# Performance work log

Hardware: AMD Instinct MI355X
Metric: run time of the kernel (lower is better)

## Reference

```python
import jax, jax.numpy as jnp
import numpy as np

CHANNELS = 256   # input_channels == output_channels == res_feature channels
HIDDEN = 128
NODES = 7

def setup_inputs() -> dict:
    key = jax.random.key(0)
    k1, k2, k3, k4, k5 = jax.random.split(key, 5)
    batch, d, h, w = 2, 16, 64, 64
    inp = jax.random.normal(k1, (1, batch, NODES, HIDDEN), dtype=jnp.float32)
    res_feature = jax.random.normal(k2, (batch, CHANNELS, d, h, w), dtype=jnp.float32)
    # xavier_uniform-style init
    def xavier(k, shape):
        fan_in, fan_out = shape[0], shape[1]
        a = jnp.sqrt(6.0 / (fan_in + fan_out))
        return jax.random.uniform(k, shape, dtype=jnp.float32, minval=-a, maxval=a)
    node_fea_for_res = xavier(k3, (CHANNELS, NODES))
    node_fea_for_hidden = xavier(k4, (HIDDEN, 1))
    weight = xavier(k5, (HIDDEN, CHANNELS))
    return {"inp": inp, "res_feature": res_feature,
            "node_fea_for_res": node_fea_for_res,
            "node_fea_for_hidden": node_fea_for_hidden,
            "weight": weight}

def reference(inp, res_feature, node_fea_for_res, node_fea_for_hidden, weight):
    b, c, d, h, w = res_feature.shape
    # [b, dhw, c]
    rf = res_feature.reshape(b, c, d * h * w).transpose(0, 2, 1)
    # scores from residual features: [b, dhw, nodes]
    n1 = rf @ node_fea_for_res
    # scores from node hidden features (constant over spatial dim): [b, nodes]
    # (original expands input over dhw then matmuls with [hidden,1]; equivalent)
    n2 = (inp[0] @ node_fea_for_hidden)[..., 0]
    attn = jax.nn.softmax(n1 + n2[:, None, :], axis=-1)  # [b, dhw, nodes]
    new_weight = inp[0] @ weight                          # [b, nodes, c]
    feature_out = jnp.einsum('bpn,bnc->bpc', attn, new_weight)  # [b, dhw, c]
    feature_out = feature_out.transpose(0, 2, 1).reshape(b, c, d, h, w)
    return jax.nn.relu(feature_out)
```

## Files before the change

kernel.cpp:

```cpp
#include <hip/hip_runtime.h>

#define DHW    65536
#define NCH    256
#define NNODE  7
#define NHID   128
#define NBATCH 2

__global__ void prep_kernel(const float* __restrict__ inp,
                            const float* __restrict__ nfh,
                            const float* __restrict__ weight,
                            const float* __restrict__ w1,
                            float* __restrict__ nwt,
                            float* __restrict__ n2g,
                            float* __restrict__ w1p)
{
    const int bn = blockIdx.x;
    const int b  = bn / NNODE;
    const int n  = bn % NNODE;
    const int t  = threadIdx.x;
    const float* ih = inp + (b * NNODE + n) * NHID;

    float acc = 0.f;
    #pragma unroll 8
    for (int h = 0; h < NHID; ++h)
        acc = fmaf(ih[h], weight[h * NCH + t], acc);
    nwt[(b * NCH + t) * 8 + n] = acc;

    if (bn == 0) {
        #pragma unroll
        for (int n2 = 0; n2 < NNODE; ++n2) w1p[t * 8 + n2] = w1[t * NNODE + n2];
        w1p[t * 8 + 7] = 0.f;
    }

    __shared__ float red[NHID];
    if (t < NHID) red[t] = ih[t] * nfh[t];
    __syncthreads();
    for (int s = NHID / 2; s > 0; s >>= 1) {
        if (t < s) red[t] += red[t + s];
        __syncthreads();
    }
    if (t == 0) n2g[b * 8 + n] = red[0];
}

__global__ __launch_bounds__(256, 8)
void main_kernel(const float* __restrict__ rf,
                 const float* __restrict__ w1p,
                 const float* __restrict__ nwt,
                 const float* __restrict__ n2g,
                 float* __restrict__ out)
{
    __shared__ float red[8][4][64];

    const int t    = threadIdx.x;
    const int lane = t & 63;
    const int wv   = __builtin_amdgcn_readfirstlane(t >> 6);
    const int blk  = blockIdx.x;
    const int b    = blk >> 10;
    const int p    = ((blk & 1023) << 6) + lane;
    const int c0   = wv << 6;

    const float*  rp = rf + ((size_t)b << 24) + ((size_t)c0 << 16) + p;
    const float4* wq = (const float4*)w1p + (c0 << 1);

    float s0 = 0.f, s1 = 0.f, s2 = 0.f, s3 = 0.f, s4 = 0.f, s5 = 0.f, s6 = 0.f;
    #pragma unroll 8
    for (int c = 0; c < 64; ++c) {
        float  v  = rp[(size_t)c << 16];
        float4 wa = wq[c * 2];
        float4 wb = wq[c * 2 + 1];
        s0 = fmaf(v, wa.x, s0);
        s1 = fmaf(v, wa.y, s1);
        s2 = fmaf(v, wa.z, s2);
        s3 = fmaf(v, wa.w, s3);
        s4 = fmaf(v, wb.x, s4);
        s5 = fmaf(v, wb.y, s5);
        s6 = fmaf(v, wb.z, s6);
    }

    red[0][wv][lane] = s0;  red[1][wv][lane] = s1;  red[2][wv][lane] = s2;
    red[3][wv][lane] = s3;  red[4][wv][lane] = s4;  red[5][wv][lane] = s5;
    red[6][wv][lane] = s6;
    __syncthreads();

    const float* n2 = n2g + b * 8;
    float r0 = red[0][0][lane] + red[0][1][lane] + red[0][2][lane] + red[0][3][lane] + n2[0];
    float r1 = red[1][0][lane] + red[1][1][lane] + red[1][2][lane] + red[1][3][lane] + n2[1];
    float r2 = red[2][0][lane] + red[2][1][lane] + red[2][2][lane] + red[2][3][lane] + n2[2];
    float r3 = red[3][0][lane] + red[3][1][lane] + red[3][2][lane] + red[3][3][lane] + n2[3];
    float r4 = red[4][0][lane] + red[4][1][lane] + red[4][2][lane] + red[4][3][lane] + n2[4];
    float r5 = red[5][0][lane] + red[5][1][lane] + red[5][2][lane] + red[5][3][lane] + n2[5];
    float r6 = red[6][0][lane] + red[6][1][lane] + red[6][2][lane] + red[6][3][lane] + n2[6];

    float m = fmaxf(fmaxf(fmaxf(r0, r1), fmaxf(r2, r3)),
                    fmaxf(fmaxf(r4, r5), r6));
    float e0 = __expf(r0 - m), e1 = __expf(r1 - m), e2 = __expf(r2 - m);
    float e3 = __expf(r3 - m), e4 = __expf(r4 - m), e5 = __expf(r5 - m);
    float e6 = __expf(r6 - m);
    float inv = 1.0f / (e0 + e1 + e2 + e3 + e4 + e5 + e6);
    float a0 = e0 * inv, a1 = e1 * inv, a2 = e2 * inv, a3 = e3 * inv;
    float a4 = e4 * inv, a5 = e5 * inv, a6 = e6 * inv;

    const float4* nq = (const float4*)nwt + ((b * NCH + c0) << 1);
    float* op = out + ((size_t)b << 24) + ((size_t)c0 << 16) + p;
    #pragma unroll 8
    for (int c = 0; c < 64; ++c) {
        float4 na = nq[c * 2];
        float4 nb = nq[c * 2 + 1];
        float o = a0 * na.x + a1 * na.y + a2 * na.z + a3 * na.w
                + a4 * nb.x + a5 * nb.y + a6 * nb.z;
        op[(size_t)c << 16] = fmaxf(o, 0.f);
    }
}

extern "C" void kernel_launch(void* const* d_in, const int* in_sizes, int n_in,
                              void* d_out, int out_size, void* d_ws, size_t ws_size,
                              hipStream_t stream) {
    const float* inp = (const float*)d_in[0];
    const float* rf  = (const float*)d_in[1];
    const float* w1  = (const float*)d_in[2];
    const float* nfh = (const float*)d_in[3];
    const float* wgt = (const float*)d_in[4];
    float* out = (float*)d_out;

    float* nwt = (float*)d_ws;
    float* n2g = nwt + NBATCH * NCH * 8;
    float* w1p = n2g + NBATCH * 8;

    prep_kernel<<<NBATCH * NNODE, 256, 0, stream>>>(inp, nfh, wgt, w1, nwt, n2g, w1p);
    main_kernel<<<NBATCH * 1024, 256, 0, stream>>>(rf, w1p, nwt, n2g, out);
}
```

Measured before the change: 266.2 us.

## Split fused kernel into score, softmax and output passes with float4 access

The single fused kernel, which reduced per-pixel scores across channel waves in shared memory, is replaced by three kernels. One computes partial node scores per channel chunk into a global buffer, one reduces them and applies the softmax into an attention buffer, and one writes the output. All kernels use float4 loads and stores, with each thread handling 4 pixels. This adds roughly 2x extra intermediate global traffic (partials plus attention, about 6 MB written and read) and two more launches, in exchange for wider memory accesses and no block-level synchronisation.

```diff
diff --git a/kernel.cpp b/kernel.cpp
--- a/kernel.cpp
+++ b/kernel.cpp
@@ -5,6 +5,30 @@
 #define NNODE  7
 #define NHID   128
 #define NBATCH 2
+#define CCH    64
+#define NCC    4
+#define PTILE  1024
+
+__device__ inline float4 f4fma(float4 v, float w, float4 a) {
+    a.x = fmaf(v.x, w, a.x); a.y = fmaf(v.y, w, a.y);
+    a.z = fmaf(v.z, w, a.z); a.w = fmaf(v.w, w, a.w);
+    return a;
+}
+__device__ inline float4 f4max(float4 a, float4 b) {
+    return make_float4(fmaxf(a.x,b.x), fmaxf(a.y,b.y), fmaxf(a.z,b.z), fmaxf(a.w,b.w));
+}
+__device__ inline float4 f4expsub(float4 a, float4 m) {
+    return make_float4(__expf(a.x-m.x), __expf(a.y-m.y), __expf(a.z-m.z), __expf(a.w-m.w));
+}
+__device__ inline float4 f4add(float4 a, float4 b) {
+    return make_float4(a.x+b.x, a.y+b.y, a.z+b.z, a.w+b.w);
+}
+__device__ inline float4 f4mul(float4 a, float4 b) {
+    return make_float4(a.x*b.x, a.y*b.y, a.z*b.z, a.w*b.w);
+}
+__device__ inline float4 f4relu(float4 a) {
+    return make_float4(fmaxf(a.x,0.f), fmaxf(a.y,0.f), fmaxf(a.z,0.f), fmaxf(a.w,0.f));
+}
 
 __global__ void prep_kernel(const float* __restrict__ inp,
                             const float* __restrict__ nfh,
@@ -28,7 +52,7 @@
 
     if (bn == 0) {
         #pragma unroll
-        for (int n2 = 0; n2 < NNODE; ++n2) w1p[t * 8 + n2] = w1[t * NNODE + n2];
+        for (int k = 0; k < NNODE; ++k) w1p[t * 8 + k] = w1[t * NNODE + k];
         w1p[t * 8 + 7] = 0.f;
     }
 
@@ -42,73 +66,112 @@
     if (t == 0) n2g[b * 8 + n] = red[0];
 }
 
-__global__ __launch_bounds__(256, 8)
-void main_kernel(const float* __restrict__ rf,
-                 const float* __restrict__ w1p,
-                 const float* __restrict__ nwt,
-                 const float* __restrict__ n2g,
-                 float* __restrict__ out)
+__global__ __launch_bounds__(256, 2)
+void score_kernel(const float* __restrict__ rf,
+                  const float* __restrict__ w1p,
+                  float* __restrict__ partial)
 {
-    __shared__ float red[8][4][64];
+    const int blk = blockIdx.x;
+    const int pc  = blk & 63;
+    const int cc  = (blk >> 6) & (NCC - 1);
+    const int b   = blk >> 8;
+    const int t   = threadIdx.x;
+    const int i4  = pc * 256 + t;
+    const int c0  = cc * CCH;
 
-    const int t    = threadIdx.x;
-    const int lane = t & 63;
-    const int wv   = __builtin_amdgcn_readfirstlane(t >> 6);
-    const int blk  = blockIdx.x;
-    const int b    = blk >> 10;
-    const int p    = ((blk & 1023) << 6) + lane;
-    const int c0   = wv << 6;
-
-    const float*  rp = rf + ((size_t)b << 24) + ((size_t)c0 << 16) + p;
+    const float4* rp = (const float4*)rf + (((size_t)(b * NCH + c0)) << 14) + i4;
     const float4* wq = (const float4*)w1p + (c0 << 1);
 
-    float s0 = 0.f, s1 = 0.f, s2 = 0.f, s3 = 0.f, s4 = 0.f, s5 = 0.f, s6 = 0.f;
+    float4 a0 = {0,0,0,0}, a1 = {0,0,0,0}, a2 = {0,0,0,0}, a3 = {0,0,0,0};
+    float4 a4 = {0,0,0,0}, a5 = {0,0,0,0}, a6 = {0,0,0,0};
+
     #pragma unroll 8
-    for (int c = 0; c < 64; ++c) {
-        float  v  = rp[(size_t)c << 16];
-        float4 wa = wq[c * 2];
-        float4 wb = wq[c * 2 + 1];
-        s0 = fmaf(v, wa.x, s0);
-        s1 = fmaf(v, wa.y, s1);
-        s2 = fmaf(v, wa.z, s2);
-        s3 = fmaf(v, wa.w, s3);
-        s4 = fmaf(v, wb.x, s4);
-        s5 = fmaf(v, wb.y, s5);
-        s6 = fmaf(v, wb.z, s6);
+    for (int ci = 0; ci < CCH; ++ci) {
+        float4 v  = rp[(size_t)ci << 14];
+        float4 wa = wq[ci * 2];
+        float4 wb = wq[ci * 2 + 1];
+        a0 = f4fma(v, wa.x, a0);
+        a1 = f4fma(v, wa.y, a1);
+        a2 = f4fma(v, wa.z, a2);
+        a3 = f4fma(v, wa.w, a3);
+        a4 = f4fma(v, wb.x, a4);
+        a5 = f4fma(v, wb.y, a5);
+        a6 = f4fma(v, wb.z, a6);
     }
 
-    red[0][wv][lane] = s0;  red[1][wv][lane] = s1;  red[2][wv][lane] = s2;
-    red[3][wv][lane] = s3;  red[4][wv][lane] = s4;  red[5][wv][lane] = s5;
-    red[6][wv][lane] = s6;
-    __syncthreads();
+    float4* pp = (float4*)partial + (((b * NCC + cc) * 8) << 14) + i4;
+    pp[0 << 14] = a0;  pp[1 << 14] = a1;  pp[2 << 14] = a2;  pp[3 << 14] = a3;
+    pp[4 << 14] = a4;  pp[5 << 14] = a5;  pp[6 << 14] = a6;
+}
 
-    const float* n2 = n2g + b * 8;
-    float r0 = red[0][0][lane] + red[0][1][lane] + red[0][2][lane] + red[0][3][lane] + n2[0];
-    float r1 = red[1][0][lane] + red[1][1][lane] + red[1][2][lane] + red[1][3][lane] + n2[1];
-    float r2 = red[2][0][lane] + red[2][1][lane] + red[2][2][lane] + red[2][3][lane] + n2[2];
-    float r3 = red[3][0][lane] + red[3][1][lane] + red[3][2][lane] + red[3][3][lane] + n2[3];
-    float r4 = red[4][0][lane] + red[4][1][lane] + red[4][2][lane] + red[4][3][lane] + n2[4];
-    float r5 = red[5][0][lane] + red[5][1][lane] + red[5][2][lane] + red[5][3][lane] + n2[5];
-    float r6 = red[6][0][lane] + red[6][1][lane] + red[6][2][lane] + red[6][3][lane] + n2[6];
+__global__ void softmax_kernel(const float* __restrict__ partial,
+                               const float* __restrict__ n2g,
+                               float* __restrict__ attn)
+{
+    const int g  = blockIdx.x * 256 + threadIdx.x;
+    const int b  = g >> 14;
+    const int i4 = g & 16383;
 
-    float m = fmaxf(fmaxf(fmaxf(r0, r1), fmaxf(r2, r3)),
-                    fmaxf(fmaxf(r4, r5), r6));
-    float e0 = __expf(r0 - m), e1 = __expf(r1 - m), e2 = __expf(r2 - m);
-    float e3 = __expf(r3 - m), e4 = __expf(r4 - m), e5 = __expf(r5 - m);
-    float e6 = __expf(r6 - m);
-    float inv = 1.0f / (e0 + e1 + e2 + e3 + e4 + e5 + e6);
-    float a0 = e0 * inv, a1 = e1 * inv, a2 = e2 * inv, a3 = e3 * inv;
-    float a4 = e4 * inv, a5 = e5 * inv, a6 = e6 * inv;
+    const float4* pp = (const float4*)partial + (((size_t)b * NCC * 8) << 14) + i4;
+    const float*  n2 = n2g + b * 8;
+
+    float4 s[NNODE];
+    #pragma unroll
+    for (int n = 0; n < NNODE; ++n) {
+        float4 acc = make_float4(n2[n], n2[n], n2[n], n2[n]);
+        #pragma unroll
+        for (int cc = 0; cc < NCC; ++cc)
+            acc = f4add(acc, pp[(size_t)((cc * 8 + n)) << 14]);
+        s[n] = acc;
+    }
+    float4 m = s[0];
+    #pragma unroll
+    for (int n = 1; n < NNODE; ++n) m = f4max(m, s[n]);
+    float4 e[NNODE];
+    float4 sum = {0,0,0,0};
+    #pragma unroll
+    for (int n = 0; n < NNODE; ++n) { e[n] = f4expsub(s[n], m); sum = f4add(sum, e[n]); }
+    float4 inv = make_float4(1.f/sum.x, 1.f/sum.y, 1.f/sum.z, 1.f/sum.w);
+
+    float4* ap = (float4*)attn + (((size_t)b * 8) << 14) + i4;
+    #pragma unroll
+    for (int n = 0; n < NNODE; ++n) ap[(size_t)n << 14] = f4mul(e[n], inv);
+}
+
+__global__ __launch_bounds__(256, 2)
+void out_kernel(const float* __restrict__ attn,
+                const float* __restrict__ nwt,
+                float* __restrict__ out)
+{
+    const int blk = blockIdx.x;
+    const int pc  = blk & 63;
+    const int cc  = (blk >> 6) & (NCC - 1);
+    const int b   = blk >> 8;
+    const int t   = threadIdx.x;
+    const int i4  = pc * 256 + t;
+    const int c0  = cc * CCH;
+
+    const float4* ap = (const float4*)attn + (((size_t)b * 8) << 14) + i4;
+    float4 a[NNODE];
+    #pragma unroll
+    for (int n = 0; n < NNODE; ++n) a[n] = ap[(size_t)n << 14];
 
     const float4* nq = (const float4*)nwt + ((b * NCH + c0) << 1);
-    float* op = out + ((size_t)b << 24) + ((size_t)c0 << 16) + p;
+    float4* op = (float4*)out + (((size_t)(b * NCH + c0)) << 14) + i4;
+
     #pragma unroll 8
-    for (int c = 0; c < 64; ++c) {
-        float4 na = nq[c * 2];
-        float4 nb = nq[c * 2 + 1];
-        float o = a0 * na.x + a1 * na.y + a2 * na.z + a3 * na.w
-                + a4 * nb.x + a5 * nb.y + a6 * nb.z;
-        op[(size_t)c << 16] = fmaxf(o, 0.f);
+    for (int ci = 0; ci < CCH; ++ci) {
+        float4 na = nq[ci * 2];
+        float4 nb = nq[ci * 2 + 1];
+        float4 o = {0,0,0,0};
+        o = f4fma(a[0], na.x, o);
+        o = f4fma(a[1], na.y, o);
+        o = f4fma(a[2], na.z, o);
+        o = f4fma(a[3], na.w, o);
+        o = f4fma(a[4], nb.x, o);
+        o = f4fma(a[5], nb.y, o);
+        o = f4fma(a[6], nb.z, o);
+        op[(size_t)ci << 14] = f4relu(o);
     }
 }
 
@@ -122,10 +185,14 @@
     const float* wgt = (const float*)d_in[4];
     float* out = (float*)d_out;
 
-    float* nwt = (float*)d_ws;
-    float* n2g = nwt + NBATCH * NCH * 8;
-    float* w1p = n2g + NBATCH * 8;
+    float* partial = (float*)d_ws;
+    float* attn    = partial + (size_t)NBATCH*NCC*8*DHW;
+    float* nwt     = attn    + (size_t)NBATCH*8*DHW;
+    float* n2g     = nwt     + NBATCH*NCH*8;
+    float* w1p     = n2g     + NBATCH*8;
 
     prep_kernel<<<NBATCH * NNODE, 256, 0, stream>>>(inp, nfh, wgt, w1, nwt, n2g, w1p);
-    main_kernel<<<NBATCH * 1024, 256, 0, stream>>>(rf, w1p, nwt, n2g, out);
+    score_kernel<<<NBATCH * NCC * 64, 256, 0, stream>>>(rf, w1p, partial);
+    softmax_kernel<<<128, 256, 0, stream>>>(partial, n2g, attn);
+    out_kernel<<<NBATCH * NCC * 64, 256, 0, stream>>>(attn, nwt, out);
 }
```

Result: no change. 270.0 us (+1.4%).

## Process four spatial positions per thread with vector and nontemporal loads/stores

Applied to the files above, without the earlier changes.

Each thread now handles four consecutive spatial positions using 16-byte vector loads of the residual features and 16-byte stores of the output. Both use nontemporal hints to avoid polluting cache with streaming data. The grid shrinks 4x, the launch-bound occupancy hint drops to 2 blocks, and shared memory grows to hold float4 partial scores. This is meant to cut memory instruction count and raise bytes per request on a bandwidth-bound kernel, at the cost of higher register use and fewer resident waves for latency hiding.

```diff
diff --git a/kernel.cpp b/kernel.cpp
--- a/kernel.cpp
+++ b/kernel.cpp
@@ -5,6 +5,14 @@
 #define NNODE  7
 #define NHID   128
 #define NBATCH 2
+
+typedef float vf4 __attribute__((ext_vector_type(4)));
+
+__device__ inline float4 f4fma(float4 v, float w, float4 a) {
+    a.x = fmaf(v.x, w, a.x); a.y = fmaf(v.y, w, a.y);
+    a.z = fmaf(v.z, w, a.z); a.w = fmaf(v.w, w, a.w);
+    return a;
+}
 
 __global__ void prep_kernel(const float* __restrict__ inp,
                             const float* __restrict__ nfh,
@@ -28,7 +36,7 @@
 
     if (bn == 0) {
         #pragma unroll
-        for (int n2 = 0; n2 < NNODE; ++n2) w1p[t * 8 + n2] = w1[t * NNODE + n2];
+        for (int k = 0; k < NNODE; ++k) w1p[t * 8 + k] = w1[t * NNODE + k];
         w1p[t * 8 + 7] = 0.f;
     }
 
@@ -42,73 +50,100 @@
     if (t == 0) n2g[b * 8 + n] = red[0];
 }
 
-__global__ __launch_bounds__(256, 8)
+__global__ __launch_bounds__(256, 2)
 void main_kernel(const float* __restrict__ rf,
                  const float* __restrict__ w1p,
                  const float* __restrict__ nwt,
                  const float* __restrict__ n2g,
                  float* __restrict__ out)
 {
-    __shared__ float red[8][4][64];
+    __shared__ float4 red[NNODE][4][64];
 
     const int t    = threadIdx.x;
     const int lane = t & 63;
     const int wv   = __builtin_amdgcn_readfirstlane(t >> 6);
     const int blk  = blockIdx.x;
-    const int b    = blk >> 10;
-    const int p    = ((blk & 1023) << 6) + lane;
+    const int b    = blk >> 8;
+    const int i4   = ((blk & 255) << 6) + lane;
     const int c0   = wv << 6;
 
-    const float*  rp = rf + ((size_t)b << 24) + ((size_t)c0 << 16) + p;
+    const vf4* rp = (const vf4*)rf + (((size_t)(b * NCH + c0)) << 14) + i4;
     const float4* wq = (const float4*)w1p + (c0 << 1);
 
-    float s0 = 0.f, s1 = 0.f, s2 = 0.f, s3 = 0.f, s4 = 0.f, s5 = 0.f, s6 = 0.f;
+    float4 a0 = {0,0,0,0}, a1 = {0,0,0,0}, a2 = {0,0,0,0}, a3 = {0,0,0,0};
+    float4 a4 = {0,0,0,0}, a5 = {0,0,0,0}, a6 = {0,0,0,0};
+
     #pragma unroll 8
-    for (int c = 0; c < 64; ++c) {
-        float  v  = rp[(size_t)c << 16];
-        float4 wa = wq[c * 2];
-        float4 wb = wq[c * 2 + 1];
-        s0 = fmaf(v, wa.x, s0);
-        s1 = fmaf(v, wa.y, s1);
-        s2 = fmaf(v, wa.z, s2);
-        s3 = fmaf(v, wa.w, s3);
-        s4 = fmaf(v, wb.x, s4);
-        s5 = fmaf(v, wb.y, s5);
-        s6 = fmaf(v, wb.z, s6);
+    for (int ci = 0; ci < 64; ++ci) {
+        vf4 vv = __builtin_nontemporal_load(&rp[(size_t)ci << 14]);
+        float4 v = make_float4(vv.x, vv.y, vv.z, vv.w);
+        float4 wa = wq[ci * 2];
+        float4 wb = wq[ci * 2 + 1];
+        a0 = f4fma(v, wa.x, a0);
+        a1 = f4fma(v, wa.y, a1);
+        a2 = f4fma(v, wa.z, a2);
+        a3 = f4fma(v, wa.w, a3);
+        a4 = f4fma(v, wb.x, a4);
+        a5 = f4fma(v, wb.y, a5);
+        a6 = f4fma(v, wb.z, a6);
     }
 
-    red[0][wv][lane] = s0;  red[1][wv][lane] = s1;  red[2][wv][lane] = s2;
-    red[3][wv][lane] = s3;  red[4][wv][lane] = s4;  red[5][wv][lane] = s5;
-    red[6][wv][lane] = s6;
+    red[0][wv][lane] = a0;  red[1][wv][lane] = a1;  red[2][wv][lane] = a2;
+    red[3][wv][lane] = a3;  red[4][wv][lane] = a4;  red[5][wv][lane] = a5;
+    red[6][wv][lane] = a6;
     __syncthreads();
 
     const float* n2 = n2g + b * 8;
-    float r0 = red[0][0][lane] + red[0][1][lane] + red[0][2][lane] + red[0][3][lane] + n2[0];
-    float r1 = red[1][0][lane] + red[1][1][lane] + red[1][2][lane] + red[1][3][lane] + n2[1];
-    float r2 = red[2][0][lane] + red[2][1][lane] + red[2][2][lane] + red[2][3][lane] + n2[2];
-    float r3 = red[3][0][lane] + red[3][1][lane] + red[3][2][lane] + red[3][3][lane] + n2[3];
-    float r4 = red[4][0][lane] + red[4][1][lane] + red[4][2][lane] + red[4][3][lane] + n2[4];
-    float r5 = red[5][0][lane] + red[5][1][lane] + red[5][2][lane] + red[5][3][lane] + n2[5];
-    float r6 = red[6][0][lane] + red[6][1][lane] + red[6][2][lane] + red[6][3][lane] + n2[6];
-
-    float m = fmaxf(fmaxf(fmaxf(r0, r1), fmaxf(r2, r3)),
-                    fmaxf(fmaxf(r4, r5), r6));
-    float e0 = __expf(r0 - m), e1 = __expf(r1 - m), e2 = __expf(r2 - m);
-    float e3 = __expf(r3 - m), e4 = __expf(r4 - m), e5 = __expf(r5 - m);
-    float e6 = __expf(r6 - m);
-    float inv = 1.0f / (e0 + e1 + e2 + e3 + e4 + e5 + e6);
-    float a0 = e0 * inv, a1 = e1 * inv, a2 = e2 * inv, a3 = e3 * inv;
-    float a4 = e4 * inv, a5 = e5 * inv, a6 = e6 * inv;
+    float4 s[NNODE];
+    #pragma unroll
+    for (int n = 0; n < NNODE; ++n) {
+        float4 r = red[n][0][lane];
+        #pragma unroll
+        for (int w = 1; w < 4; ++w) {
+            float4 q = red[n][w][lane];
+            r.x += q.x; r.y += q.y; r.z += q.z; r.w += q.w;
+        }
+        r.x += n2[n]; r.y += n2[n]; r.z += n2[n]; r.w += n2[n];
+        s[n] = r;
+    }
+    float4 m = s[0];
+    #pragma unroll
+    for (int n = 1; n < NNODE; ++n) {
+        m.x = fmaxf(m.x, s[n].x); m.y = fmaxf(m.y, s[n].y);
+        m.z = fmaxf(m.z, s[n].z); m.w = fmaxf(m.w, s[n].w);
+    }
+    float4 sum = {0,0,0,0};
+    float4 e[NNODE];
+    #pragma unroll
+    for (int n = 0; n < NNODE; ++n) {
+        e[n].x = __expf(s[n].x - m.x); e[n].y = __expf(s[n].y - m.y);
+        e[n].z = __expf(s[n].z - m.z); e[n].w = __expf(s[n].w - m.w);
+        sum.x += e[n].x; sum.y += e[n].y; sum.z += e[n].z; sum.w += e[n].w;
+    }
+    float4 inv = make_float4(1.f/sum.x, 1.f/sum.y, 1.f/sum.z, 1.f/sum.w);
+    #pragma unroll
+    for (int n = 0; n < NNODE; ++n) {
+        e[n].x *= inv.x; e[n].y *= inv.y; e[n].z *= inv.z; e[n].w *= inv.w;
+    }
 
     const float4* nq = (const float4*)nwt + ((b * NCH + c0) << 1);
-    float* op = out + ((size_t)b << 24) + ((size_t)c0 << 16) + p;
+    vf4* op = (vf4*)out + (((size_t)(b * NCH + c0)) << 14) + i4;
     #pragma unroll 8
-    for (int c = 0; c < 64; ++c) {
-        float4 na = nq[c * 2];
-        float4 nb = nq[c * 2 + 1];
-        float o = a0 * na.x + a1 * na.y + a2 * na.z + a3 * na.w
-                + a4 * nb.x + a5 * nb.y + a6 * nb.z;
-        op[(size_t)c << 16] = fmaxf(o, 0.f);
+    for (int ci = 0; ci < 64; ++ci) {
+        float4 na = nq[ci * 2];
+        float4 nb = nq[ci * 2 + 1];
+        float4 o = {0,0,0,0};
+        o = f4fma(e[0], na.x, o);
+        o = f4fma(e[1], na.y, o);
+        o = f4fma(e[2], na.z, o);
+        o = f4fma(e[3], na.w, o);
+        o = f4fma(e[4], nb.x, o);
+        o = f4fma(e[5], nb.y, o);
+        o = f4fma(e[6], nb.z, o);
+        vf4 ov;
+        ov.x = fmaxf(o.x, 0.f); ov.y = fmaxf(o.y, 0.f);
+        ov.z = fmaxf(o.z, 0.f); ov.w = fmaxf(o.w, 0.f);
+        __builtin_nontemporal_store(ov, &op[(size_t)ci << 14]);
     }
 }
 
@@ -127,5 +162,5 @@
     float* w1p = n2g + NBATCH * 8;
 
     prep_kernel<<<NBATCH * NNODE, 256, 0, stream>>>(inp, nfh, wgt, w1, nwt, n2g, w1p);
-    main_kernel<<<NBATCH * 1024, 256, 0, stream>>>(rf, w1p, nwt, n2g, out);
+    main_kernel<<<NBATCH * 256, 256, 0, stream>>>(rf, w1p, nwt, n2g, out);
 }
```

Result: faster. 245.3 us (-7.8%).
